# Kernel optimization log

Hardware: AMD Instinct MI355X
Metric: run time of the kernel (lower is better)

The kernel has to match this reference:

```python
import jax, jax.numpy as jnp
import numpy as np
from jax import lax

T, B, F, U = 512, 256, 128, 128


def setup_inputs() -> dict:
    key = jax.random.key(0)
    k1, k2, k3, k4, k5 = jax.random.split(key, 5)
    inputs = jax.random.normal(k1, (T, B, F), dtype=jnp.float32)
    states = jax.random.normal(k2, (2, B, U), dtype=jnp.float32)
    dones = (jax.random.uniform(k3, (T, B)) < 0.1).astype(jnp.float32)
    kernelx = jax.random.normal(k4, (F, 4 * U), dtype=jnp.float32) / np.sqrt(F)
    kernelh = jax.random.normal(k5, (U, 4 * U), dtype=jnp.float32) / np.sqrt(U)
    bias = jnp.zeros((4 * U,), dtype=jnp.float32)  # created but unused in original call()
    return {"inputs": inputs, "states": states, "dones": dones,
            "kernelx": kernelx, "kernelh": kernelh, "bias": bias}


def reference(inputs, states, dones, kernelx, kernelh, bias):
    # inputs: [T, B, F]; states: [2, B, U]; dones: [T, B]
    c0, h0 = states[0], states[1]
    masks = (1.0 - dones)[..., None]  # [T, B, 1]

    def step(carry, xm):
        c, h = carry
        x, m = xm
        c = c * m
        h = h * m
        z = x @ kernelx + h @ kernelh  # [B, 4U]; NB: original never adds bias
        i, f, o, u = jnp.split(z, 4, axis=1)
        i = jax.nn.sigmoid(i)
        f = jax.nn.sigmoid(f)
        o = jax.nn.sigmoid(o)
        u = jnp.tanh(u)
        c = f * c + i * u
        h = o * jnp.tanh(c)
        return (c, h), h

    (c, h), outputs = lax.scan(step, (c0, h0), (inputs, masks))
    return outputs, jnp.stack([c, h])
```

## Files before the change

kernel.cpp:

```cpp
#include <hip/hip_runtime.h>

#define T_  512
#define B_  256
#define F_  128
#define U_  128
#define G4_ 512
#define L2E 1.4426950408889634f
#define NBLK 32
#define ZSTR8 (16 * 512 * 8)
#define ZB_BYTES ((size_t)T_ * B_ * G4_ * 2)

using f32x4 = __attribute__((ext_vector_type(4))) float;
using f32x2 = __attribute__((ext_vector_type(2))) float;
using s16x8 = __attribute__((ext_vector_type(8))) short;
using u32x4 = __attribute__((ext_vector_type(4))) unsigned int;

#if __has_builtin(__builtin_amdgcn_exp2f)
#define EXP2(x) __builtin_amdgcn_exp2f(x)
#else
#define EXP2(x) exp2f(x)
#endif

__device__ __forceinline__ unsigned fbits(float f) { return __builtin_bit_cast(unsigned, f); }
__device__ __forceinline__ float bitsf(unsigned u) { return __builtin_bit_cast(float, u); }

__device__ __forceinline__ unsigned short f2bf(float f) {
  unsigned u = fbits(f);
  u += 0x7FFFu + ((u >> 16) & 1u);
  return (unsigned short)(u >> 16);
}
__device__ __forceinline__ unsigned cvt_pk_bf16(float lo, float hi) {
  unsigned r;
  asm("v_cvt_pk_bf16_f32 %0, %1, %2" : "=v"(r) : "v"(lo), "v"(hi));
  return r;
}
__device__ __forceinline__ s16x8 pack8(f32x4 a, f32x4 b) {
  u32x4 w;
  w[0] = cvt_pk_bf16(a[0], a[1]);
  w[1] = cvt_pk_bf16(a[2], a[3]);
  w[2] = cvt_pk_bf16(b[0], b[1]);
  w[3] = cvt_pk_bf16(b[2], b[3]);
  return __builtin_bit_cast(s16x8, w);
}
__device__ __forceinline__ void sync_lds() {
  asm volatile("s_waitcnt lgkmcnt(0)\n\ts_barrier" ::: "memory");
}

__global__ __launch_bounds__(512, 1)
void zxb_gemm_kernel(const float* __restrict__ X, const float* __restrict__ WX,
                     unsigned* __restrict__ ZB)
{
  const int tid  = threadIdx.x;
  const int w    = tid >> 6;
  const int lane = tid & 63;
  const int lr   = lane & 15;
  const int lk   = lane >> 4;

  s16x8 bWx[4][4];
#pragma unroll
  for (int g = 0; g < 4; ++g) {
    const float scl = (g == 3) ? 2.0f * L2E : L2E;
    const int col = g * 128 + w * 16 + lr;
#pragma unroll
    for (int kc = 0; kc < 4; ++kc) {
      s16x8 wx;
#pragma unroll
      for (int e = 0; e < 8; ++e) {
        const int k = kc * 32 + lk * 8 + e;
        wx[e] = (short)f2bf(WX[k * G4_ + col] * scl);
      }
      bWx[g][kc] = wx;
    }
  }

  const int G0 = blockIdx.x * 32;
  const float* xp = X + (size_t)(G0 * 16 + lr) * F_ + lk * 8;
  unsigned*    zp = ZB + ((size_t)(G0 * 8 + w) * 64 + lane) * 8;

  for (int grp = 0; grp < 32; ++grp) {
    s16x8 xa[4];
#pragma unroll
    for (int kc = 0; kc < 4; ++kc)
      xa[kc] = pack8(*(const f32x4*)(xp + kc * 32), *(const f32x4*)(xp + kc * 32 + 4));
#pragma unroll
    for (int g = 0; g < 4; ++g) {
      f32x4 a = {0.f, 0.f, 0.f, 0.f};
#pragma unroll
      for (int kc = 0; kc < 4; ++kc)
        a = __builtin_amdgcn_mfma_f32_16x16x32_bf16(xa[kc], bWx[g][kc], a, 0, 0, 0);
      const unsigned p0 = ((unsigned)f2bf(a[1]) << 16) | (unsigned)f2bf(a[0]);
      const unsigned p1 = ((unsigned)f2bf(a[3]) << 16) | (unsigned)f2bf(a[2]);
      zp[g * 2]     = p0;
      zp[g * 2 + 1] = p1;
    }
    xp += 16 * F_;
    zp += 8 * 64 * 8;
  }
}

__global__ __launch_bounds__(512, 1)
void lstm_zxb_kernel(const unsigned* __restrict__ ZB, const float* __restrict__ ST,
                     const float* __restrict__ DN, const float* __restrict__ WH,
                     float* __restrict__ OUT)
{
  __shared__ __align__(16) short hbuf[2][16 * U_];

  const int tid  = threadIdx.x;
  const int w    = tid >> 6;
  const int lane = tid & 63;
  const int lr   = lane & 15;
  const int lk   = lane >> 4;
  const int lkm  = lk & 1;
  const int r0   = (lk >> 1) * 2;
  const int b0   = blockIdx.x * 8;
  const int wr0  = lkm * 4 + r0;
  const int uu   = w * 16 + lr;

  const int doff2 = b0 + wr0;
  const int ooff2 = (b0 + wr0) * U_ + uu;

  const int hA0 = (wr0 + 0) * U_ + ((((uu >> 3) ^ (wr0 + 0)) & 15) * 8) + (uu & 7);
  const int hA1 = (wr0 + 1) * U_ + ((((uu >> 3) ^ (wr0 + 1)) & 15) * 8) + (uu & 7);
  const int hB0 = (wr0 + 8) * U_ + ((((uu >> 3) ^ (wr0 + 8)) & 15) * 8) + (uu & 7);
  const int hB1 = (wr0 + 9) * U_ + ((((uu >> 3) ^ (wr0 + 9)) & 15) * 8) + (uu & 7);

  s16x8 bWh[4][4];
#pragma unroll
  for (int g = 0; g < 4; ++g) {
    const float scl = (g == 3) ? 2.0f * L2E : L2E;
    const int col = g * 128 + uu;
#pragma unroll
    for (int kc = 0; kc < 4; ++kc) {
      s16x8 wh;
#pragma unroll
      for (int e = 0; e < 8; ++e) {
        const int k = kc * 32 + lk * 8 + e;
        wh[e] = (short)f2bf(WH[k * G4_ + col] * scl);
      }
      bWh[g][kc] = wh;
    }
  }

  float c[2], hn[2];
  c[0]  = ST[(doff2 + 0) * U_ + uu];
  c[1]  = ST[(doff2 + 1) * U_ + uu];
  hn[0] = ST[(B_ + doff2 + 0) * U_ + uu];
  hn[1] = ST[(B_ + doff2 + 1) * U_ + uu];
  {
    f32x2 d2 = *(const f32x2*)&DN[doff2];
    const float m0 = 1.0f - d2[0], m1 = 1.0f - d2[1];
    c[0] *= m0; c[1] *= m1;
    const unsigned pk = cvt_pk_bf16(hn[0] * m0, hn[1] * m1);
    hbuf[0][hA0] = (short)pk;          hbuf[0][hB0] = (short)pk;
    hbuf[0][hA1] = (short)(pk >> 16);  hbuf[0][hB1] = (short)(pk >> 16);
  }

  const int bt  = blockIdx.x >> 1;
  const int lkw = (blockIdx.x & 1) * 2 + lkm;
  const int zoff = ((bt * 8 + w) * 64 + lkw * 16 + lr) * 8;

  u32x4 zA0, zA1, zB0, zB1;
  f32x2 dv;
  zA0 = *(const u32x4*)(ZB + zoff);
  zA1 = *(const u32x4*)(ZB + zoff + 4);
  zB0 = *(const u32x4*)(ZB + ZSTR8 + zoff);
  zB1 = *(const u32x4*)(ZB + ZSTR8 + zoff + 4);
  dv = *(const f32x2*)&DN[B_ + doff2];
  sync_lds();

  auto step = [&](const int p, const bool pub, const bool pre,
                  u32x4& zq0, u32x4& zq1, const int tz, const int td, const int to) {
    s16x8 ah[4];
#pragma unroll
    for (int kc = 0; kc < 4; ++kc) {
      const int sl = (kc * 4 + lk) ^ lr;
      ah[kc] = *(const s16x8*)&hbuf[p][lr * U_ + sl * 8];
    }
    f32x4 az[4];
#pragma unroll
    for (int g = 0; g < 4; ++g) {
      const unsigned d0 = (g < 2) ? zq0[(g & 1) * 2]     : zq1[(g & 1) * 2];
      const unsigned d1 = (g < 2) ? zq0[(g & 1) * 2 + 1] : zq1[(g & 1) * 2 + 1];
      f32x4 a = { bitsf(d0 << 16), bitsf(d0 & 0xFFFF0000u),
                  bitsf(d1 << 16), bitsf(d1 & 0xFFFF0000u) };
#pragma unroll
      for (int kc = 0; kc < 4; ++kc)
        a = __builtin_amdgcn_mfma_f32_16x16x32_bf16(ah[kc], bWh[g][kc], a, 0, 0, 0);
      az[g] = a;
    }
    if (pre) {
      zq0 = *(const u32x4*)(ZB + tz + zoff);
      zq1 = *(const u32x4*)(ZB + tz + zoff + 4);
    }
#pragma unroll
    for (int j = 0; j < 2; ++j) {
      const int r = r0 + j;
      const float eA = EXP2(-az[0][r]);
      const float eC = EXP2(-az[1][r]);
      const float eD = EXP2(-az[2][r]);
      const float eB = EXP2(-az[3][r]);
      const float iu = (1.0f - eB) * __builtin_amdgcn_rcpf((1.0f + eA) * (1.0f + eB));
      const float fg = __builtin_amdgcn_rcpf(1.0f + eC);
      const float cn = fmaf(fg, c[j], iu);
      const float ce = fminf(fmaxf(cn, -15.0f), 15.0f);
      const float eE = EXP2(ce * (-2.0f * L2E));
      const float h  = (1.0f - eE) * __builtin_amdgcn_rcpf((1.0f + eD) * (1.0f + eE));
      c[j]  = cn;
      hn[j] = h;
      OUT[to + ooff2 + j * U_] = h;
    }
    f32x2 dcur = dv;
    if (pre) dv = *(const f32x2*)(DN + td + doff2);
    if (pub) {
      const float m0 = 1.0f - dcur[0], m1 = 1.0f - dcur[1];
      c[0] *= m0; c[1] *= m1;
      const unsigned pk = cvt_pk_bf16(hn[0] * m0, hn[1] * m1);
      short* hb = hbuf[p ^ 1];
      hb[hA0] = (short)pk;          hb[hB0] = (short)pk;
      hb[hA1] = (short)(pk >> 16);  hb[hB1] = (short)(pk >> 16);
    }
    sync_lds();
  };

  for (int t = 0; t < T_; t += 2) {
    step(0, true, t + 2 < T_, zA0, zA1,
         (t + 2) * ZSTR8, (t + 2) * B_, t * (B_ * U_));
    step(1, t + 2 < T_, t + 3 < T_, zB0, zB1,
         (t + 3) * ZSTR8, (t + 3) * B_, (t + 1) * (B_ * U_));
  }

  const long fb = (long)T_ * B_ * U_;
#pragma unroll
  for (int j = 0; j < 2; ++j) {
    OUT[fb + (long)(doff2 + j) * U_ + uu]                 = c[j];
    OUT[fb + (long)B_ * U_ + (long)(doff2 + j) * U_ + uu] = hn[j];
  }
}

__global__ __launch_bounds__(512, 1)
void lstm_fb_kernel(const float* __restrict__ X, const float* __restrict__ ST,
                    const float* __restrict__ DN, const float* __restrict__ WX,
                    const float* __restrict__ WH, float* __restrict__ OUT)
{
  __shared__ __align__(16) short hbuf[2][16 * U_];

  const int tid  = threadIdx.x;
  const int w    = tid >> 6;
  const int lane = tid & 63;
  const int lr   = lane & 15;
  const int lk   = lane >> 4;
  const int b0   = blockIdx.x * 16;
  const int row0 = lk * 4;
  const int uu   = w * 16 + lr;

  const int xoff = (b0 + lr) * F_ + lk * 8;
  const int doff = b0 + row0;
  const int ooff = (b0 + row0) * U_ + uu;

  s16x8 bWh[4][4], bWx[4][4];
#pragma unroll
  for (int g = 0; g < 4; ++g) {
    const int col = g * 128 + uu;
#pragma unroll
    for (int kc = 0; kc < 4; ++kc) {
      s16x8 wh, wx;
#pragma unroll
      for (int e = 0; e < 8; ++e) {
        const int k = kc * 32 + lk * 8 + e;
        wh[e] = (short)f2bf(WH[k * G4_ + col]);
        wx[e] = (short)f2bf(WX[k * G4_ + col]);
      }
      bWh[g][kc] = wh;
      bWx[g][kc] = wx;
    }
  }

  float c[4], hn[4];
#pragma unroll
  for (int r = 0; r < 4; ++r) {
    c[r]  = ST[(b0 + row0 + r) * U_ + uu];
    hn[r] = ST[(B_ + b0 + row0 + r) * U_ + uu];
  }
  {
    f32x4 d = *(const f32x4*)&DN[doff];
#pragma unroll
    for (int r = 0; r < 4; ++r) {
      const float m = 1.0f - d[r];
      c[r] *= m;
      const int row = row0 + r;
      const int sl  = (uu >> 3) ^ row;
      hbuf[0][row * U_ + sl * 8 + (uu & 7)] = (short)cvt_pk_bf16(hn[r] * m, 0.f);
    }
  }

  f32x4 xv0[4], xv1[4], dv;
  f32x4 accA[4], accB[4];
  {
    const float* xp = X + xoff;
    s16x8 xa[4];
#pragma unroll
    for (int kc = 0; kc < 4; ++kc)
      xa[kc] = pack8(*(const f32x4*)(xp + kc * 32), *(const f32x4*)(xp + kc * 32 + 4));
#pragma unroll
    for (int g = 0; g < 4; ++g) {
      f32x4 a = {0.f, 0.f, 0.f, 0.f};
#pragma unroll
      for (int kc = 0; kc < 4; ++kc)
        a = __builtin_amdgcn_mfma_f32_16x16x32_bf16(xa[kc], bWx[g][kc], a, 0, 0, 0);
      accA[g] = a;
    }
#pragma unroll
    for (int kc = 0; kc < 4; ++kc) {
      xv0[kc] = *(const f32x4*)(X + B_ * F_ + xoff + kc * 32);
      xv1[kc] = *(const f32x4*)(X + B_ * F_ + xoff + kc * 32 + 4);
    }
    dv = *(const f32x4*)(DN + B_ + doff);
  }
  sync_lds();

  const float* Xt  = X + 2 * B_ * F_;
  const float* DNt = DN + 2 * B_;
  float*       Ot  = OUT;

  auto step = [&](const int p, const bool act_x, const bool pre_x,
                  f32x4 (&accZ)[4], f32x4 (&accX)[4]) {
    s16x8 ah[4];
#pragma unroll
    for (int kc = 0; kc < 4; ++kc) {
      const int sl = (kc * 4 + lk) ^ lr;
      ah[kc] = *(const s16x8*)&hbuf[p][lr * U_ + sl * 8];
    }
#pragma unroll
    for (int g = 0; g < 4; ++g) {
      f32x4 a = accZ[g];
#pragma unroll
      for (int kc = 0; kc < 4; ++kc)
        a = __builtin_amdgcn_mfma_f32_16x16x32_bf16(ah[kc], bWh[g][kc], a, 0, 0, 0);
      accZ[g] = a;
    }
#pragma unroll
    for (int r = 0; r < 4; ++r) {
      const float eA = __expf(-accZ[0][r]);
      const float eB = __expf(-2.0f * accZ[3][r]);
      const float eC = __expf(-accZ[1][r]);
      const float eD = __expf(-accZ[2][r]);
      const float iu = (1.0f - eB) * __builtin_amdgcn_rcpf((1.0f + eA) * (1.0f + eB));
      const float fg = __builtin_amdgcn_rcpf(1.0f + eC);
      const float cn = fmaf(fg, c[r], iu);
      const float ce = fminf(fmaxf(cn, -30.0f), 30.0f);
      const float eE = __expf(-2.0f * ce);
      const float h  = (1.0f - eE) * __builtin_amdgcn_rcpf((1.0f + eD) * (1.0f + eE));
      c[r]  = cn;
      hn[r] = h;
      Ot[ooff + r * U_] = h;
    }
    if (act_x) {
      s16x8 xa[4];
#pragma unroll
      for (int kc = 0; kc < 4; ++kc) xa[kc] = pack8(xv0[kc], xv1[kc]);
#pragma unroll
      for (int g = 0; g < 4; ++g) {
        f32x4 a = {0.f, 0.f, 0.f, 0.f};
#pragma unroll
        for (int kc = 0; kc < 4; ++kc)
          a = __builtin_amdgcn_mfma_f32_16x16x32_bf16(xa[kc], bWx[g][kc], a, 0, 0, 0);
        accX[g] = a;
      }
    }
    f32x4 dcur = dv;
    if (pre_x) {
#pragma unroll
      for (int kc = 0; kc < 4; ++kc) {
        xv0[kc] = *(const f32x4*)(Xt + xoff + kc * 32);
        xv1[kc] = *(const f32x4*)(Xt + xoff + kc * 32 + 4);
      }
      dv = *(const f32x4*)(DNt + doff);
    }
    if (act_x) {
#pragma unroll
      for (int r = 0; r < 4; ++r) {
        const float m = 1.0f - dcur[r];
        c[r] *= m;
        const int row = row0 + r;
        const int sl  = (uu >> 3) ^ row;
        hbuf[p ^ 1][row * U_ + sl * 8 + (uu & 7)] = (short)cvt_pk_bf16(hn[r] * m, 0.f);
      }
    }
    sync_lds();
  };

  for (int t = 0; t < T_; t += 2) {
    step(0, true, t + 2 < T_, accA, accB);
    Xt += B_ * F_; DNt += B_; Ot += B_ * U_;
    step(1, t + 2 < T_, t + 3 < T_, accB, accA);
    Xt += B_ * F_; DNt += B_; Ot += B_ * U_;
  }

  const long fb = (long)T_ * B_ * U_;
#pragma unroll
  for (int r = 0; r < 4; ++r) {
    OUT[fb + (long)(b0 + row0 + r) * U_ + uu]                 = c[r];
    OUT[fb + (long)B_ * U_ + (long)(b0 + row0 + r) * U_ + uu] = hn[r];
  }
}

extern "C" void kernel_launch(void* const* d_in, const int* in_sizes, int n_in,
                              void* d_out, int out_size, void* d_ws, size_t ws_size,
                              hipStream_t stream) {
  const float* X  = (const float*)d_in[0];
  const float* ST = (const float*)d_in[1];
  const float* DN = (const float*)d_in[2];
  const float* WX = (const float*)d_in[3];
  const float* WH = (const float*)d_in[4];
  float* OUT = (float*)d_out;

  if (ws_size >= ZB_BYTES) {
    unsigned* ZB = (unsigned*)d_ws;
    zxb_gemm_kernel<<<dim3(256), dim3(512), 0, stream>>>(X, WX, ZB);
    lstm_zxb_kernel<<<dim3(NBLK), dim3(512), 0, stream>>>(ZB, ST, DN, WH, OUT);
  } else {
    lstm_fb_kernel<<<dim3(16), dim3(512), 0, stream>>>(X, ST, DN, WX, WH, OUT);
  }
}
```

Measured before the change: 460.8 us.

## Split recurrent LSTM over 64 blocks with 4 batch rows each

The recurrent kernel now assigns 4 batch rows per block instead of 8 and launches 64 blocks instead of 32, so more compute units share the serial time loop. Each lane handles one row, and its h value is replicated into four LDS rows so the 16-row MFMA tile stays filled. This halves the per-step elementwise work per block, but the MFMA count per block is unchanged and more of each 16-row tile is redundant.

```diff
diff --git a/kernel.cpp b/kernel.cpp
--- a/kernel.cpp
+++ b/kernel.cpp
@@ -6,7 +6,7 @@
 #define U_  128
 #define G4_ 512
 #define L2E 1.4426950408889634f
-#define NBLK 32
+#define NBLK 64
 #define ZSTR8 (16 * 512 * 8)
 #define ZB_BYTES ((size_t)T_ * B_ * G4_ * 2)
 
@@ -99,9 +99,9 @@
 }
 
 __global__ __launch_bounds__(512, 1)
-void lstm_zxb_kernel(const unsigned* __restrict__ ZB, const float* __restrict__ ST,
-                     const float* __restrict__ DN, const float* __restrict__ WH,
-                     float* __restrict__ OUT)
+void lstm_zxb4_kernel(const unsigned* __restrict__ ZB, const float* __restrict__ ST,
+                      const float* __restrict__ DN, const float* __restrict__ WH,
+                      float* __restrict__ OUT)
 {
   __shared__ __align__(16) short hbuf[2][16 * U_];
 
@@ -110,19 +110,17 @@
   const int lane = tid & 63;
   const int lr   = lane & 15;
   const int lk   = lane >> 4;
-  const int lkm  = lk & 1;
-  const int r0   = (lk >> 1) * 2;
-  const int b0   = blockIdx.x * 8;
-  const int wr0  = lkm * 4 + r0;
+  const int rl   = lk;
+  const int b0   = blockIdx.x * 4;
   const int uu   = w * 16 + lr;
 
-  const int doff2 = b0 + wr0;
-  const int ooff2 = (b0 + wr0) * U_ + uu;
-
-  const int hA0 = (wr0 + 0) * U_ + ((((uu >> 3) ^ (wr0 + 0)) & 15) * 8) + (uu & 7);
-  const int hA1 = (wr0 + 1) * U_ + ((((uu >> 3) ^ (wr0 + 1)) & 15) * 8) + (uu & 7);
-  const int hB0 = (wr0 + 8) * U_ + ((((uu >> 3) ^ (wr0 + 8)) & 15) * 8) + (uu & 7);
-  const int hB1 = (wr0 + 9) * U_ + ((((uu >> 3) ^ (wr0 + 9)) & 15) * 8) + (uu & 7);
+  const int doff1 = b0 + rl;
+  const int ooff1 = (b0 + rl) * U_ + uu;
+
+  const int hP0 = (rl +  0) * U_ + ((((uu >> 3) ^ (rl +  0)) & 15) * 8) + (uu & 7);
+  const int hP1 = (rl +  4) * U_ + ((((uu >> 3) ^ (rl +  4)) & 15) * 8) + (uu & 7);
+  const int hP2 = (rl +  8) * U_ + ((((uu >> 3) ^ (rl +  8)) & 15) * 8) + (uu & 7);
+  const int hP3 = (rl + 12) * U_ + ((((uu >> 3) ^ (rl + 12)) & 15) * 8) + (uu & 7);
 
   s16x8 bWh[4][4];
 #pragma unroll
@@ -141,31 +139,25 @@
     }
   }
 
-  float c[2], hn[2];
-  c[0]  = ST[(doff2 + 0) * U_ + uu];
-  c[1]  = ST[(doff2 + 1) * U_ + uu];
-  hn[0] = ST[(B_ + doff2 + 0) * U_ + uu];
-  hn[1] = ST[(B_ + doff2 + 1) * U_ + uu];
+  float c  = ST[doff1 * U_ + uu];
+  float hn = ST[(B_ + doff1) * U_ + uu];
   {
-    f32x2 d2 = *(const f32x2*)&DN[doff2];
-    const float m0 = 1.0f - d2[0], m1 = 1.0f - d2[1];
-    c[0] *= m0; c[1] *= m1;
-    const unsigned pk = cvt_pk_bf16(hn[0] * m0, hn[1] * m1);
-    hbuf[0][hA0] = (short)pk;          hbuf[0][hB0] = (short)pk;
-    hbuf[0][hA1] = (short)(pk >> 16);  hbuf[0][hB1] = (short)(pk >> 16);
-  }
-
-  const int bt  = blockIdx.x >> 1;
-  const int lkw = (blockIdx.x & 1) * 2 + lkm;
-  const int zoff = ((bt * 8 + w) * 64 + lkw * 16 + lr) * 8;
+    const float m = 1.0f - DN[doff1];
+    c *= m;
+    const unsigned short hv = f2bf(hn * m);
+    hbuf[0][hP0] = (short)hv;  hbuf[0][hP1] = (short)hv;
+    hbuf[0][hP2] = (short)hv;  hbuf[0][hP3] = (short)hv;
+  }
+
+  const int zoff = ((((int)blockIdx.x >> 2) * 8 + w) * 64 + ((int)blockIdx.x & 3) * 16 + lr) * 8;
 
   u32x4 zA0, zA1, zB0, zB1;
-  f32x2 dv;
+  float dv;
   zA0 = *(const u32x4*)(ZB + zoff);
   zA1 = *(const u32x4*)(ZB + zoff + 4);
   zB0 = *(const u32x4*)(ZB + ZSTR8 + zoff);
   zB1 = *(const u32x4*)(ZB + ZSTR8 + zoff + 4);
-  dv = *(const f32x2*)&DN[B_ + doff2];
+  dv = DN[B_ + doff1];
   sync_lds();
 
   auto step = [&](const int p, const bool pub, const bool pre,
@@ -192,32 +184,34 @@
       zq0 = *(const u32x4*)(ZB + tz + zoff);
       zq1 = *(const u32x4*)(ZB + tz + zoff + 4);
     }
-#pragma unroll
-    for (int j = 0; j < 2; ++j) {
-      const int r = r0 + j;
-      const float eA = EXP2(-az[0][r]);
-      const float eC = EXP2(-az[1][r]);
-      const float eD = EXP2(-az[2][r]);
-      const float eB = EXP2(-az[3][r]);
+    {
+      const float z0 = az[0][rl];
+      const float z1 = az[1][rl];
+      const float z2 = az[2][rl];
+      const float z3 = az[3][rl];
+      const float eA = EXP2(-z0);
+      const float eC = EXP2(-z1);
+      const float eD = EXP2(-z2);
+      const float eB = EXP2(-z3);
       const float iu = (1.0f - eB) * __builtin_amdgcn_rcpf((1.0f + eA) * (1.0f + eB));
       const float fg = __builtin_amdgcn_rcpf(1.0f + eC);
-      const float cn = fmaf(fg, c[j], iu);
+      const float cn = fmaf(fg, c, iu);
       const float ce = fminf(fmaxf(cn, -15.0f), 15.0f);
       const float eE = EXP2(ce * (-2.0f * L2E));
       const float h  = (1.0f - eE) * __builtin_amdgcn_rcpf((1.0f + eD) * (1.0f + eE));
-      c[j]  = cn;
-      hn[j] = h;
-      OUT[to + ooff2 + j * U_] = h;
-    }
-    f32x2 dcur = dv;
-    if (pre) dv = *(const f32x2*)(DN + td + doff2);
+      c  = cn;
+      hn = h;
+      OUT[to + ooff1] = h;
+    }
+    const float dcur = dv;
+    if (pre) dv = DN[td + doff1];
     if (pub) {
-      const float m0 = 1.0f - dcur[0], m1 = 1.0f - dcur[1];
-      c[0] *= m0; c[1] *= m1;
-      const unsigned pk = cvt_pk_bf16(hn[0] * m0, hn[1] * m1);
+      const float m = 1.0f - dcur;
+      c *= m;
+      const unsigned short hv = f2bf(hn * m);
       short* hb = hbuf[p ^ 1];
-      hb[hA0] = (short)pk;          hb[hB0] = (short)pk;
-      hb[hA1] = (short)(pk >> 16);  hb[hB1] = (short)(pk >> 16);
+      hb[hP0] = (short)hv;  hb[hP1] = (short)hv;
+      hb[hP2] = (short)hv;  hb[hP3] = (short)hv;
     }
     sync_lds();
   };
@@ -230,11 +224,8 @@
   }
 
   const long fb = (long)T_ * B_ * U_;
-#pragma unroll
-  for (int j = 0; j < 2; ++j) {
-    OUT[fb + (long)(doff2 + j) * U_ + uu]                 = c[j];
-    OUT[fb + (long)B_ * U_ + (long)(doff2 + j) * U_ + uu] = hn[j];
-  }
+  OUT[fb + (long)doff1 * U_ + uu]                 = c;
+  OUT[fb + (long)B_ * U_ + (long)doff1 * U_ + uu] = hn;
 }
 
 __global__ __launch_bounds__(512, 1)
@@ -417,7 +408,7 @@
   if (ws_size >= ZB_BYTES) {
     unsigned* ZB = (unsigned*)d_ws;
     zxb_gemm_kernel<<<dim3(256), dim3(512), 0, stream>>>(X, WX, ZB);
-    lstm_zxb_kernel<<<dim3(NBLK), dim3(512), 0, stream>>>(ZB, ST, DN, WH, OUT);
+    lstm_zxb4_kernel<<<dim3(NBLK), dim3(512), 0, stream>>>(ZB, ST, DN, WH, OUT);
   } else {
     lstm_fb_kernel<<<dim3(16), dim3(512), 0, stream>>>(X, ST, DN, WX, WH, OUT);
   }
```

Result: faster. 416.2 us (-9.7%).
